# Performance work log

Measured on AMD Instinct MI355X. Metric: run time of the kernel, lower is better.

The kernel has to match this reference:

```python
import jax, jax.numpy as jnp
import numpy as np

D_MODEL = 1024
N_OCTAVES = 3


def _index_maps(d_model: int, n_octaves: int):
    """Static octave index maps, matching HarmonicMixing._build_index_maps."""
    maps = []
    for octave in range(1, n_octaves + 1):
        stride = 2 ** octave
        up_src = np.arange(d_model // stride)
        up_tgt = up_src * stride                      # i -> i*stride
        down_src = np.arange(stride, d_model)
        down_tgt = down_src // stride                 # i -> i // stride (many-to-one)
        maps.append((up_src, up_tgt, down_src, down_tgt))
    return maps


def setup_inputs() -> dict:
    key = jax.random.key(0)
    k1, k2, k3 = jax.random.split(key, 3)
    x = jax.random.normal(k1, (8, 4096, D_MODEL), dtype=jnp.float32)
    up_weights = jax.random.uniform(k2, (N_OCTAVES,), dtype=jnp.float32)
    down_weights = jax.random.uniform(k3, (N_OCTAVES,), dtype=jnp.float32)
    return {"x": x, "up_weights": up_weights, "down_weights": down_weights}


def reference(x, up_weights, down_weights):
    d_model = x.shape[-1]
    maps = _index_maps(d_model, N_OCTAVES)
    out = x
    for o, (up_src, up_tgt, down_src, down_tgt) in enumerate(maps):
        up_w = jax.nn.sigmoid(up_weights[o])
        down_w = jax.nn.sigmoid(down_weights[o])
        # gather -> scale -> scatter-add (duplicate targets accumulate)
        out = out.at[..., up_tgt].add(up_w * x[..., up_src])
        out = out.at[..., down_tgt].add(down_w * x[..., down_src])
    return out
```

## Files before the change

### kernel.cpp

```cpp
#include <hip/hip_runtime.h>


constexpr int D = 1024;

__global__ __launch_bounds__(256) void harmonic_kernel(
    const float* __restrict__ x,
    const float* __restrict__ uwp,
    const float* __restrict__ dwp,
    float* __restrict__ out)
{
    __shared__ float rowlo[512];
    __shared__ float S1[512];
    __shared__ float S2[256];
    __shared__ float S3[128];

    const int t = threadIdx.x;
    const long long base = (long long)blockIdx.x * D;

    const float uw0 = 1.f / (1.f + __expf(-uwp[0]));
    const float uw1 = 1.f / (1.f + __expf(-uwp[1]));
    const float uw2 = 1.f / (1.f + __expf(-uwp[2]));
    const float dw0 = 1.f / (1.f + __expf(-dwp[0]));
    const float dw1 = 1.f / (1.f + __expf(-dwp[1]));
    const float dw2 = 1.f / (1.f + __expf(-dwp[2]));

    const int j0 = t * 4;
    const float4 v = *reinterpret_cast<const float4*>(x + base + j0);

    const float s1a = v.x + v.y;
    const float s1b = v.z + v.w;
    const float s2  = s1a + s1b;
    const float s3  = s2 + __shfl_xor(s2, 1);

    if (t < 128) *reinterpret_cast<float4*>(&rowlo[j0]) = v;
    *reinterpret_cast<float2*>(&S1[2 * t]) = make_float2(s1a, s1b);
    S2[t] = s2;
    if ((t & 1) == 0) S3[t >> 1] = s3;
    __syncthreads();

    float4 r = v;

    const float2 u01 = *reinterpret_cast<const float2*>(&rowlo[2 * t]);
    r.x += uw0 * u01.x;
    r.z += uw0 * u01.y;
    r.x += uw1 * rowlo[t];
    if ((t & 1) == 0) r.x += uw2 * rowlo[t >> 1];

    if (t < 128) {
        const float4 a = *reinterpret_cast<const float4*>(&S1[j0]);
        if (t > 0) r.x += dw0 * a.x;
        r.y += dw0 * a.y;
        r.z += dw0 * a.z;
        r.w += dw0 * a.w;
        if (t < 64) {
            const float4 b = *reinterpret_cast<const float4*>(&S2[j0]);
            if (t > 0) r.x += dw1 * b.x;
            r.y += dw1 * b.y;
            r.z += dw1 * b.z;
            r.w += dw1 * b.w;
            if (t < 32) {
                const float4 c = *reinterpret_cast<const float4*>(&S3[j0]);
                if (t > 0) r.x += dw2 * c.x;
                r.y += dw2 * c.y;
                r.z += dw2 * c.z;
                r.w += dw2 * c.w;
            }
        }
    }

    *reinterpret_cast<float4*>(out + base + j0) = r;
}

extern "C" void kernel_launch(void* const* d_in, const int* in_sizes, int n_in,
                              void* d_out, int out_size, void* d_ws, size_t ws_size,
                              hipStream_t stream) {
    const float* x   = (const float*)d_in[0];
    const float* uwp = (const float*)d_in[1];
    const float* dwp = (const float*)d_in[2];
    float* out = (float*)d_out;
    const int n_rows = in_sizes[0] / D;
    harmonic_kernel<<<n_rows, 256, 0, stream>>>(x, uwp, dwp, out);
}
```

Before: 220.2 us.

## Process four rows per block with nontemporal vector loads and stores

Each block now handles four rows instead of one, so all four float4 loads are issued before the shared-memory phase. This amortizes the sigmoid setup and block scheduling across rows and raises memory-level parallelism. Global loads and stores now use nontemporal builtins to avoid cache pollution in this streaming kernel, and the launch bounds request more resident waves. A tail launch covers leftover rows, but the larger shared footprint and register use may lower occupancy.

New measurement: 223.3 us. No clear change (+1.4%).

```diff
diff --git a/kernel.cpp b/kernel.cpp
--- a/kernel.cpp
+++ b/kernel.cpp
@@ -3,19 +3,22 @@
 
 constexpr int D = 1024;
 
-__global__ __launch_bounds__(256) void harmonic_kernel(
+using f4 = __attribute__((ext_vector_type(4))) float;
+
+template <int R>
+__global__ __launch_bounds__(256, 7) void harmonic_kernel(
     const float* __restrict__ x,
     const float* __restrict__ uwp,
     const float* __restrict__ dwp,
     float* __restrict__ out)
 {
-    __shared__ float rowlo[512];
-    __shared__ float S1[512];
-    __shared__ float S2[256];
-    __shared__ float S3[128];
+    __shared__ float rowlo[R][512];
+    __shared__ float S1[R][512];
+    __shared__ float S2[R][256];
+    __shared__ float S3[R][128];
 
     const int t = threadIdx.x;
-    const long long base = (long long)blockIdx.x * D;
+    const long long base = (long long)blockIdx.x * R * D;
 
     const float uw0 = 1.f / (1.f + __expf(-uwp[0]));
     const float uw1 = 1.f / (1.f + __expf(-uwp[1]));
@@ -25,50 +28,63 @@
     const float dw2 = 1.f / (1.f + __expf(-dwp[2]));
 
     const int j0 = t * 4;
-    const float4 v = *reinterpret_cast<const float4*>(x + base + j0);
 
-    const float s1a = v.x + v.y;
-    const float s1b = v.z + v.w;
-    const float s2  = s1a + s1b;
-    const float s3  = s2 + __shfl_xor(s2, 1);
+    f4 v[R];
+#pragma unroll
+    for (int r = 0; r < R; ++r) {
+        v[r] = __builtin_nontemporal_load(
+            reinterpret_cast<const f4*>(x + base + (long long)r * D + j0));
+    }
 
-    if (t < 128) *reinterpret_cast<float4*>(&rowlo[j0]) = v;
-    *reinterpret_cast<float2*>(&S1[2 * t]) = make_float2(s1a, s1b);
-    S2[t] = s2;
-    if ((t & 1) == 0) S3[t >> 1] = s3;
+#pragma unroll
+    for (int r = 0; r < R; ++r) {
+        const float s1a = v[r].x + v[r].y;
+        const float s1b = v[r].z + v[r].w;
+        const float s2  = s1a + s1b;
+        const float s3  = s2 + __shfl_xor(s2, 1);
+
+        if (t < 128) *reinterpret_cast<f4*>(&rowlo[r][j0]) = v[r];
+        *reinterpret_cast<float2*>(&S1[r][2 * t]) = make_float2(s1a, s1b);
+        S2[r][t] = s2;
+        if ((t & 1) == 0) S3[r][t >> 1] = s3;
+    }
     __syncthreads();
 
-    float4 r = v;
+#pragma unroll
+    for (int r = 0; r < R; ++r) {
+        f4 o = v[r];
 
-    const float2 u01 = *reinterpret_cast<const float2*>(&rowlo[2 * t]);
-    r.x += uw0 * u01.x;
-    r.z += uw0 * u01.y;
-    r.x += uw1 * rowlo[t];
-    if ((t & 1) == 0) r.x += uw2 * rowlo[t >> 1];
+        const float2 u01 = *reinterpret_cast<const float2*>(&rowlo[r][2 * t]);
+        o.x += uw0 * u01.x;
+        o.z += uw0 * u01.y;
+        o.x += uw1 * rowlo[r][t];
+        if ((t & 1) == 0) o.x += uw2 * rowlo[r][t >> 1];
 
-    if (t < 128) {
-        const float4 a = *reinterpret_cast<const float4*>(&S1[j0]);
-        if (t > 0) r.x += dw0 * a.x;
-        r.y += dw0 * a.y;
-        r.z += dw0 * a.z;
-        r.w += dw0 * a.w;
-        if (t < 64) {
-            const float4 b = *reinterpret_cast<const float4*>(&S2[j0]);
-            if (t > 0) r.x += dw1 * b.x;
-            r.y += dw1 * b.y;
-            r.z += dw1 * b.z;
-            r.w += dw1 * b.w;
-            if (t < 32) {
-                const float4 c = *reinterpret_cast<const float4*>(&S3[j0]);
-                if (t > 0) r.x += dw2 * c.x;
-                r.y += dw2 * c.y;
-                r.z += dw2 * c.z;
-                r.w += dw2 * c.w;
+        if (t < 128) {
+            const f4 a = *reinterpret_cast<const f4*>(&S1[r][j0]);
+            if (t > 0) o.x += dw0 * a.x;
+            o.y += dw0 * a.y;
+            o.z += dw0 * a.z;
+            o.w += dw0 * a.w;
+            if (t < 64) {
+                const f4 b = *reinterpret_cast<const f4*>(&S2[r][j0]);
+                if (t > 0) o.x += dw1 * b.x;
+                o.y += dw1 * b.y;
+                o.z += dw1 * b.z;
+                o.w += dw1 * b.w;
+                if (t < 32) {
+                    const f4 c = *reinterpret_cast<const f4*>(&S3[r][j0]);
+                    if (t > 0) o.x += dw2 * c.x;
+                    o.y += dw2 * c.y;
+                    o.z += dw2 * c.z;
+                    o.w += dw2 * c.w;
+                }
             }
         }
+
+        __builtin_nontemporal_store(
+            o, reinterpret_cast<f4*>(out + base + (long long)r * D + j0));
     }
-
-    *reinterpret_cast<float4*>(out + base + j0) = r;
 }
 
 extern "C" void kernel_launch(void* const* d_in, const int* in_sizes, int n_in,
@@ -79,5 +95,11 @@
     const float* dwp = (const float*)d_in[2];
     float* out = (float*)d_out;
     const int n_rows = in_sizes[0] / D;
-    harmonic_kernel<<<n_rows, 256, 0, stream>>>(x, uwp, dwp, out);
+    const int nb  = n_rows / 4;
+    const int rem = n_rows % 4;
+    if (nb)
+        harmonic_kernel<4><<<nb, 256, 0, stream>>>(x, uwp, dwp, out);
+    if (rem)
+        harmonic_kernel<1><<<rem, 256, 0, stream>>>(
+            x + (long long)nb * 4 * D, uwp, dwp, out + (long long)nb * 4 * D);
 }
```

## Process one row per wavefront with persistent grid and double-buffered row loads

Applied to the files above, without the earlier changes.

Each 64-lane wavefront now handles a whole row, using per-wave LDS slices, so the block-wide __syncthreads barrier goes away. The grid is capped at 1792 blocks that grid-stride over rows, and the next row is loaded into a second register buffer while the current one is processed. Loads and stores use nontemporal hints, and octave-3 sums are rebuilt from S2 instead of a separate array. The cost is higher register pressure and the absence of any explicit wave-level sync between LDS writes and reads, which relies on lockstep execution within a wavefront.

Result: slower. 243.6 us (+10.6%).

```diff
diff --git a/kernel.cpp b/kernel.cpp
--- a/kernel.cpp
+++ b/kernel.cpp
@@ -3,19 +3,22 @@
 
 constexpr int D = 1024;
 
-__global__ __launch_bounds__(256) void harmonic_kernel(
+using f4 = __attribute__((ext_vector_type(4))) float;
+
+__global__ __launch_bounds__(256, 7) void harmonic_kernel(
     const float* __restrict__ x,
     const float* __restrict__ uwp,
     const float* __restrict__ dwp,
-    float* __restrict__ out)
+    float* __restrict__ out,
+    const int n_rows)
 {
-    __shared__ float rowlo[512];
-    __shared__ float S1[512];
-    __shared__ float S2[256];
-    __shared__ float S3[128];
+    __shared__ float rowlo[4][512];
+    __shared__ float S1lds[4][512];
+    __shared__ float S2lds[4][256];
 
     const int t = threadIdx.x;
-    const long long base = (long long)blockIdx.x * D;
+    const int w = t >> 6;
+    const int l = t & 63;
 
     const float uw0 = 1.f / (1.f + __expf(-uwp[0]));
     const float uw1 = 1.f / (1.f + __expf(-uwp[1]));
@@ -24,51 +27,85 @@
     const float dw1 = 1.f / (1.f + __expf(-dwp[1]));
     const float dw2 = 1.f / (1.f + __expf(-dwp[2]));
 
-    const int j0 = t * 4;
-    const float4 v = *reinterpret_cast<const float4*>(x + base + j0);
+    float* const RL = rowlo[w];
+    float* const P1 = S1lds[w];
+    float* const P2 = S2lds[w];
 
-    const float s1a = v.x + v.y;
-    const float s1b = v.z + v.w;
-    const float s2  = s1a + s1b;
-    const float s3  = s2 + __shfl_xor(s2, 1);
+    auto loadrow = [&](f4* v, const float* p) {
+#pragma unroll
+        for (int m = 0; m < 4; ++m)
+            v[m] = __builtin_nontemporal_load(reinterpret_cast<const f4*>(p + 256 * m));
+    };
 
-    if (t < 128) *reinterpret_cast<float4*>(&rowlo[j0]) = v;
-    *reinterpret_cast<float2*>(&S1[2 * t]) = make_float2(s1a, s1b);
-    S2[t] = s2;
-    if ((t & 1) == 0) S3[t >> 1] = s3;
-    __syncthreads();
+    auto process = [&](f4* v, float* po) {
+        *reinterpret_cast<f4*>(&RL[4 * l])       = v[0];
+        *reinterpret_cast<f4*>(&RL[256 + 4 * l]) = v[1];
+#pragma unroll
+        for (int m = 0; m < 4; ++m) {
+            const float s1a = v[m].x + v[m].y;
+            const float s1b = v[m].z + v[m].w;
+            *reinterpret_cast<float2*>(&P1[128 * m + 2 * l]) = make_float2(s1a, s1b);
+            P2[64 * m + l] = s1a + s1b;
+        }
 
-    float4 r = v;
+#pragma unroll
+        for (int m = 0; m < 4; ++m) {
+            const float2 u = *reinterpret_cast<const float2*>(&RL[128 * m + 2 * l]);
+            v[m].x += uw0 * u.x;
+            v[m].z += uw0 * u.y;
+            v[m].x += uw1 * RL[64 * m + l];
+            if ((l & 1) == 0) v[m].x += uw2 * RL[32 * m + (l >> 1)];
+        }
 
-    const float2 u01 = *reinterpret_cast<const float2*>(&rowlo[2 * t]);
-    r.x += uw0 * u01.x;
-    r.z += uw0 * u01.y;
-    r.x += uw1 * rowlo[t];
-    if ((t & 1) == 0) r.x += uw2 * rowlo[t >> 1];
+#pragma unroll
+        for (int m = 0; m < 2; ++m) {
+            const f4 a = *reinterpret_cast<const f4*>(&P1[256 * m + 4 * l]);
+            if (m > 0 || l > 0) v[m].x += dw0 * a.x;
+            v[m].y += dw0 * a.y;
+            v[m].z += dw0 * a.z;
+            v[m].w += dw0 * a.w;
+        }
+        {
+            const f4 b = *reinterpret_cast<const f4*>(&P2[4 * l]);
+            if (l > 0) v[0].x += dw1 * b.x;
+            v[0].y += dw1 * b.y;
+            v[0].z += dw1 * b.z;
+            v[0].w += dw1 * b.w;
+        }
+        if (l < 32) {
+            const f4 p = *reinterpret_cast<const f4*>(&P2[8 * l]);
+            const f4 q = *reinterpret_cast<const f4*>(&P2[8 * l + 4]);
+            if (l > 0) v[0].x += dw2 * (p.x + p.y);
+            v[0].y += dw2 * (p.z + p.w);
+            v[0].z += dw2 * (q.x + q.y);
+            v[0].w += dw2 * (q.z + q.w);
+        }
 
-    if (t < 128) {
-        const float4 a = *reinterpret_cast<const float4*>(&S1[j0]);
-        if (t > 0) r.x += dw0 * a.x;
-        r.y += dw0 * a.y;
-        r.z += dw0 * a.z;
-        r.w += dw0 * a.w;
-        if (t < 64) {
-            const float4 b = *reinterpret_cast<const float4*>(&S2[j0]);
-            if (t > 0) r.x += dw1 * b.x;
-            r.y += dw1 * b.y;
-            r.z += dw1 * b.z;
-            r.w += dw1 * b.w;
-            if (t < 32) {
-                const float4 c = *reinterpret_cast<const float4*>(&S3[j0]);
-                if (t > 0) r.x += dw2 * c.x;
-                r.y += dw2 * c.y;
-                r.z += dw2 * c.z;
-                r.w += dw2 * c.w;
-            }
-        }
+#pragma unroll
+        for (int m = 0; m < 4; ++m)
+            __builtin_nontemporal_store(v[m], reinterpret_cast<f4*>(po + 256 * m));
+    };
+
+    const long long rowstep = 4LL * gridDim.x;
+    long long row = 4LL * blockIdx.x + w;
+    if (row >= n_rows) return;
+
+    f4 vA[4], vB[4];
+    loadrow(vA, x + row * D + 4 * l);
+    for (;;) {
+        const long long rowB = row + rowstep;
+        const bool hasB = rowB < n_rows;
+        if (hasB) loadrow(vB, x + rowB * D + 4 * l);
+        process(vA, out + row * D + 4 * l);
+        if (!hasB) return;
+
+        const long long rowC = rowB + rowstep;
+        const bool hasC = rowC < n_rows;
+        if (hasC) loadrow(vA, x + rowC * D + 4 * l);
+        process(vB, out + rowB * D + 4 * l);
+        if (!hasC) return;
+        row = rowC;
     }
-
-    *reinterpret_cast<float4*>(out + base + j0) = r;
 }
 
 extern "C" void kernel_launch(void* const* d_in, const int* in_sizes, int n_in,
@@ -79,5 +116,7 @@
     const float* dwp = (const float*)d_in[2];
     float* out = (float*)d_out;
     const int n_rows = in_sizes[0] / D;
-    harmonic_kernel<<<n_rows, 256, 0, stream>>>(x, uwp, dwp, out);
+    int ngroups = (n_rows + 3) / 4;
+    int nb = ngroups < 1792 ? ngroups : 1792;
+    harmonic_kernel<<<nb, 256, 0, stream>>>(x, uwp, dwp, out, n_rows);
 }
```
